# Optimization experiments

Hardware: AMD Instinct MI355X
Metric: run time of the kernel (lower is better)

## Reference

```python
import jax, jax.numpy as jnp
import numpy as np

B, LQ, LK, D = 16, 2048, 2048, 64
EPS = 1e-13
KEEP_PROB = 0.8  # fraction of key positions kept in the mask


def setup_inputs() -> dict:
    key = jax.random.key(0)
    kq, kk, kv, km = jax.random.split(key, 4)
    q = jax.random.normal(kq, (B, LQ, D), dtype=jnp.float32)
    k = jax.random.normal(kk, (B, LK, D), dtype=jnp.float32)
    v = jax.random.normal(kv, (B, LK, D), dtype=jnp.float32)
    # binary 0/1 float mask over key positions (ESIM-style padding mask)
    v_mask = (jax.random.uniform(km, (B, LK)) < KEEP_PROB).astype(jnp.float32)
    return {"q": q, "k": k, "v": v, "v_mask": v_mask}


def masked_softmax(scores, mask):
    # ESIM masked_softmax: softmax(scores * mask) * mask, renormalized.
    m = mask[:, None, :]  # [B, 1, Lk] broadcast over query dim
    p = jax.nn.softmax(scores * m, axis=-1) * m
    return p / (jnp.sum(p, axis=-1, keepdims=True) + EPS)


def reference(q, k, v, v_mask):
    scores = jnp.einsum("bqd,bkd->bqk", q, k)  # [B, Lq, Lk]
    attend = masked_softmax(scores, v_mask)
    return jnp.einsum("bqk,bkd->bqd", attend, v)  # [B, Lq, D]
```

## Files before the change

kernel.cpp:

```cpp
#include <hip/hip_runtime.h>
#include <hip/hip_bf16.h>
#include <stdint.h>

#define NB 16
#define SLQ 2048
#define SLK 2048
#define DD 64
#define BQ 128
#define BK 64
#define NT (SLK / BK)
#define QTILES (SLQ / BQ)
#define LOG2E 1.44269504f

typedef _Float16 f16x8 __attribute__((ext_vector_type(8)));
typedef short s16x8 __attribute__((ext_vector_type(8)));
typedef float f32x4 __attribute__((ext_vector_type(4)));
typedef float f32x2 __attribute__((ext_vector_type(2)));
typedef float f32x16 __attribute__((ext_vector_type(16)));

typedef __attribute__((address_space(1))) const void gvoid;
typedef __attribute__((address_space(3))) void lvoid;

__device__ __forceinline__ int swzb(int row, int bytecol) {
    return row * 128 + (bytecol ^ ((row & 7) << 4));
}
__device__ __forceinline__ int ldsq(int row, int bytecol) {
    return (row >> 6) * 8192 + swzb(row & 63, bytecol);
}

__device__ __forceinline__ void gload16(const void* g, void* l) {
    __builtin_amdgcn_global_load_lds((gvoid*)g, (lvoid*)l, 16, 0, 0);
}

__device__ __forceinline__ uint16_t f2bf(float f) {
    __bf16 h = (__bf16)f;
    return __builtin_bit_cast(uint16_t, h);
}
__device__ __forceinline__ float bf2f(uint16_t u) {
    uint32_t x = ((uint32_t)u) << 16;
    return __builtin_bit_cast(float, x);
}

__global__ __launch_bounds__(256)
void prep_all(const float* __restrict__ q, const float* __restrict__ k,
              const float* __restrict__ v, const float* __restrict__ vm,
              char* __restrict__ qs, char* __restrict__ ks,
              char* __restrict__ vts, float* __restrict__ bias2) {
    const int bid = blockIdx.x;
    if (bid < 1024) {
        const int tl = bid & 511;
        const bool isq = bid < 512;
        const float sc = isq ? LOG2E : 1.0f;
        const float* src = (isq ? q : k) + (size_t)tl * (BK * DD);
        char* dst = (isq ? qs : ks) + (size_t)tl * (BK * DD * 2);
        #pragma unroll
        for (int it = 0; it < 2; ++it) {
            int c = threadIdx.x + it * 256;
            int row = c >> 3, col8 = c & 7;
            f32x4 a  = *(const f32x4*)(src + row * DD + col8 * 8);
            f32x4 b2 = *(const f32x4*)(src + row * DD + col8 * 8 + 4);
            f16x8 h;
            #pragma unroll
            for (int j = 0; j < 4; ++j) {
                h[j] = (_Float16)(a[j] * sc);
                h[4 + j] = (_Float16)(b2[j] * sc);
            }
            *(f16x8*)(dst + swzb(row, col8 * 16)) = h;
        }
    } else if (bid < 1536) {
        const int tl = bid - 1024;
        const float* src = v + (size_t)tl * (BK * DD);
        char* dst = vts + (size_t)tl * (BK * DD * 2);
        const int d = threadIdx.x & 63;
        #pragma unroll
        for (int it = 0; it < 2; ++it) {
            int key8 = (threadIdx.x >> 6) + it * 4;
            s16x8 h;
            #pragma unroll
            for (int j = 0; j < 8; ++j)
                h[j] = (short)f2bf(src[(key8 * 8 + j) * DD + d]);
            *(s16x8*)(dst + swzb(d, key8 * 16)) = h;
        }
    } else {
        int i = (bid - 1536) * 256 + threadIdx.x;
        bias2[i] = (vm[i] != 0.f) ? 0.f : -2e30f;
    }
}

__global__ __launch_bounds__(256, 3)
void attn_fwd(const char* __restrict__ qs, const char* __restrict__ ks,
              const char* __restrict__ vts, const float* __restrict__ bias2,
              float* __restrict__ po, float* __restrict__ pl,
              float* __restrict__ out, int nsp)
{
    __shared__ __align__(16) char lp[BQ * DD * 2];
    __shared__ __align__(16) char lk[2][BK * DD * 2];
    __shared__ __align__(16) char lv[2][BK * DD * 2];

    const int tid  = threadIdx.x;
    const int lane = tid & 63;
    const int w    = tid >> 6;
    const int lh   = lane >> 5;
    const int lr   = lane & 31;

    const int G = 256 * nsp;
    int wg = blockIdx.x;
    wg = (wg & 7) * (G >> 3) + (wg >> 3);
    const int qt   = wg & 15;
    const int rest = wg >> 4;
    const int sp   = rest % nsp;
    const int b    = rest / nsp;

    const int qq = NT / nsp, rm = NT % nsp;
    const int t0  = sp * qq + (sp < rm ? sp : rm);
    const int cnt = qq + (sp < rm ? 1 : 0);

    const char* qtile = qs  + (size_t)(b * 32 + qt * 2) * 8192;
    const char* kbase = ks  + (size_t)(b * 32 + t0) * 8192;
    const char* vbase = vts + (size_t)(b * 32 + t0) * 8192;
    const float* mbias = bias2 + (size_t)b * SLK + t0 * BK;

    #pragma unroll
    for (int i = 0; i < 4; ++i) {
        int ch = w * 4 + i;
        gload16(qtile + ch * 1024 + lane * 16, lp + ch * 1024);
    }
    #pragma unroll
    for (int i = 0; i < 2; ++i) {
        int ch = w * 2 + i;
        gload16(kbase + ch * 1024 + lane * 16, lk[0] + ch * 1024);
        gload16(vbase + ch * 1024 + lane * 16, lv[0] + ch * 1024);
    }
    asm volatile("s_waitcnt vmcnt(0)" ::: "memory");
    __syncthreads();

    f16x8 qf[4];
    #pragma unroll
    for (int kd = 0; kd < 4; ++kd)
        qf[kd] = *(const f16x8*)(lp + ldsq(w * 32 + lr, kd * 32 + lh * 16));

    s16x8 ones;
    #pragma unroll
    for (int j = 0; j < 8; ++j) ones[j] = (short)0x3F80;

    f32x16 oacc0 = (f32x16)(0.0f), oacc1 = (f32x16)(0.0f), rsacc = (f32x16)(0.0f);

    int buf = 0;
    for (int kt = 0; kt < cnt; ++kt) {
        float bv0 = mbias[kt * BK + lr];
        float bv1 = mbias[kt * BK + 32 + lr];

        if (kt + 1 < cnt) {
            const char* kg = kbase + (size_t)(kt + 1) * 8192;
            const char* vg = vbase + (size_t)(kt + 1) * 8192;
            #pragma unroll
            for (int i = 0; i < 2; ++i) {
                int ch = w * 2 + i;
                gload16(kg + ch * 1024 + lane * 16, lk[buf ^ 1] + ch * 1024);
                gload16(vg + ch * 1024 + lane * 16, lv[buf ^ 1] + ch * 1024);
            }
        }

        f32x16 s0 = (f32x16)(0.0f), s1 = (f32x16)(0.0f);
        #pragma unroll
        for (int kd = 0; kd < 4; ++kd) {
            f16x8 kf0 = *(const f16x8*)(lk[buf] + swzb(lr,      kd * 32 + lh * 16));
            f16x8 kf1 = *(const f16x8*)(lk[buf] + swzb(32 + lr, kd * 32 + lh * 16));
            s0 = __builtin_amdgcn_mfma_f32_32x32x16_f16(qf[kd], kf0, s0, 0, 0, 0);
            s1 = __builtin_amdgcn_mfma_f32_32x32x16_f16(qf[kd], kf1, s1, 0, 0, 0);
        }

        #pragma unroll
        for (int r = 0; r < 16; ++r) {
            int row = w * 32 + (r & 3) + 8 * (r >> 2) + 4 * lh;
            float p0 = exp2f(s0[r] + bv0);
            float p1 = exp2f(s1[r] + bv1);
            *(uint16_t*)(lp + ldsq(row, lr * 2))      = f2bf(p0);
            *(uint16_t*)(lp + ldsq(row, 64 + lr * 2)) = f2bf(p1);
        }

        s16x8 pa[4];
        #pragma unroll
        for (int kk = 0; kk < 4; ++kk) {
            pa[kk] = *(const s16x8*)(lp + ldsq(w * 32 + lr, kk * 32 + lh * 16));
            rsacc = __builtin_amdgcn_mfma_f32_32x32x16_bf16(pa[kk], ones, rsacc, 0, 0, 0);
        }
        #pragma unroll
        for (int kk = 0; kk < 4; ++kk) {
            s16x8 vf0 = *(const s16x8*)(lv[buf] + swzb(lr,      kk * 32 + lh * 16));
            s16x8 vf1 = *(const s16x8*)(lv[buf] + swzb(32 + lr, kk * 32 + lh * 16));
            oacc0 = __builtin_amdgcn_mfma_f32_32x32x16_bf16(pa[kk], vf0, oacc0, 0, 0, 0);
            oacc1 = __builtin_amdgcn_mfma_f32_32x32x16_bf16(pa[kk], vf1, oacc1, 0, 0, 0);
        }

        asm volatile("s_waitcnt vmcnt(0)" ::: "memory");
        __syncthreads();
        buf ^= 1;
    }

    if (nsp == 1) {
        float* ob = out + ((size_t)b * SLQ + (size_t)qt * BQ) * DD;
        #pragma unroll
        for (int r = 0; r < 16; ++r) {
            int row = w * 32 + (r & 3) + 8 * (r >> 2) + 4 * lh;
            float inv = 1.f / (rsacc[r] + 1e-13f);
            ob[row * DD + lr]      = oacc0[r] * inv;
            ob[row * DD + 32 + lr] = oacc1[r] * inv;
        }
    } else {
        float* pob = po + (size_t)wg * (BQ * DD);
        #pragma unroll
        for (int r = 0; r < 16; ++r) {
            int row = w * 32 + (r & 3) + 8 * (r >> 2) + 4 * lh;
            pob[row * DD + lr]      = oacc0[r];
            pob[row * DD + 32 + lr] = oacc1[r];
            if (lr == 0) pl[(size_t)wg * BQ + row] = rsacc[r];
        }
    }
}

__global__ __launch_bounds__(256)
void merge_k(const float* __restrict__ po, const float* __restrict__ pl,
             float* __restrict__ out, int nsp) {
    const int t  = blockIdx.x;
    const int b  = t >> 4, qt = t & 15;
    const int i0 = (b * nsp) * 16 + qt;
    const int r0 = threadIdx.x >> 4;
    const int c4 = (threadIdx.x & 15) * 4;
    float* ob = out + ((size_t)b * SLQ + (size_t)qt * BQ) * DD;
    for (int rr = 0; rr < BQ; rr += 16) {
        int r = r0 + rr;
        float l = 1e-13f;
        f32x4 acc = (f32x4){0.f, 0.f, 0.f, 0.f};
        for (int s = 0; s < nsp; ++s) {
            int idx = i0 + s * 16;
            l += pl[(size_t)idx * BQ + r];
            f32x4 a = *(const f32x4*)(po + (size_t)idx * (BQ * DD) + r * DD + c4);
            acc += a;
        }
        float inv = 1.f / l;
        f32x4 o;
        #pragma unroll
        for (int j = 0; j < 4; ++j) o[j] = acc[j] * inv;
        *(f32x4*)(ob + r * DD + c4) = o;
    }
}

__global__ __launch_bounds__(256, 2)
void attn_fallback(const float* __restrict__ q, const float* __restrict__ k,
                   const float* __restrict__ v, const float* __restrict__ vm,
                   float* __restrict__ out)
{
    __shared__ __align__(16) char lqh[64 * DD * 2];
    __shared__ __align__(16) char lql[64 * DD * 2];
    __shared__ __align__(16) char lkh[BK * DD * 2];
    __shared__ __align__(16) char lkl[BK * DD * 2];
    __shared__ __align__(16) char lvt[DD * BK * 2];
    __shared__ __align__(16) char lpp[64 * BK * 2];
    __shared__ float lmask[BK];

    const int tid  = threadIdx.x;
    const int lane = tid & 63;
    const int w    = tid >> 6;
    const int lg   = lane >> 4;
    const int lm   = lane & 15;

    const int b  = blockIdx.y;
    const int qt = blockIdx.x;

    const float* qb = q + ((size_t)b * SLQ + (size_t)qt * 64) * DD;
    const float* kb = k + (size_t)b * SLK * DD;
    const float* vb = v + (size_t)b * SLK * DD;
    const float* mb = vm + (size_t)b * SLK;

    #pragma unroll
    for (int it = 0; it < 2; ++it) {
        int c = tid + it * 256;
        int row = c >> 3, col8 = c & 7;
        f32x4 a  = *(const f32x4*)(qb + row * DD + col8 * 8);
        f32x4 bb = *(const f32x4*)(qb + row * DD + col8 * 8 + 4);
        s16x8 h, l;
        #pragma unroll
        for (int j = 0; j < 4; ++j) {
            uint16_t hh = f2bf(a[j]);
            h[j] = (short)hh; l[j] = (short)f2bf(a[j] - bf2f(hh));
            uint16_t hb = f2bf(bb[j]);
            h[4 + j] = (short)hb; l[4 + j] = (short)f2bf(bb[j] - bf2f(hb));
        }
        *(s16x8*)(lqh + swzb(row, col8 * 16)) = h;
        *(s16x8*)(lql + swzb(row, col8 * 16)) = l;
    }
    __syncthreads();

    s16x8 qfh[2], qfl[2];
    #pragma unroll
    for (int kc = 0; kc < 2; ++kc) {
        qfh[kc] = *(const s16x8*)(lqh + swzb(w * 16 + lm, kc * 64 + lg * 16));
        qfl[kc] = *(const s16x8*)(lql + swzb(w * 16 + lm, kc * 64 + lg * 16));
    }

    float mrow[4], lrow[4];
    f32x4 oacc[4];
    #pragma unroll
    for (int i = 0; i < 4; ++i) { mrow[i] = -1e30f; lrow[i] = 0.f; }
    #pragma unroll
    for (int d = 0; d < 4; ++d) oacc[d] = (f32x4){0.f, 0.f, 0.f, 0.f};

    for (int kt = 0; kt < NT; ++kt) {
        __syncthreads();
        const float* ks2 = kb + (size_t)kt * BK * DD;
        const float* vs = vb + (size_t)kt * BK * DD;

        #pragma unroll
        for (int it = 0; it < 2; ++it) {
            int c = tid + it * 256;
            int row = c >> 3, col8 = c & 7;
            f32x4 a  = *(const f32x4*)(ks2 + row * DD + col8 * 8);
            f32x4 bb = *(const f32x4*)(ks2 + row * DD + col8 * 8 + 4);
            s16x8 h, l;
            #pragma unroll
            for (int j = 0; j < 4; ++j) {
                uint16_t hh = f2bf(a[j]);
                h[j] = (short)hh; l[j] = (short)f2bf(a[j] - bf2f(hh));
                uint16_t hb = f2bf(bb[j]);
                h[4 + j] = (short)hb; l[4 + j] = (short)f2bf(bb[j] - bf2f(hb));
            }
            *(s16x8*)(lkh + swzb(row, col8 * 16)) = h;
            *(s16x8*)(lkl + swzb(row, col8 * 16)) = l;
        }
        #pragma unroll
        for (int it = 0; it < 8; ++it) {
            int c = tid + it * 256;
            int key = c >> 5, dp = (c & 31) * 2;
            f32x2 a = *(const f32x2*)(vs + key * DD + dp);
            *(uint16_t*)(lvt + swzb(dp,     key * 2)) = f2bf(a[0]);
            *(uint16_t*)(lvt + swzb(dp + 1, key * 2)) = f2bf(a[1]);
        }
        if (tid < BK) lmask[tid] = mb[kt * BK + tid];
        __syncthreads();

        f32x4 s[4];
        #pragma unroll
        for (int f = 0; f < 4; ++f) s[f] = (f32x4){0.f, 0.f, 0.f, 0.f};
        #pragma unroll
        for (int f = 0; f < 4; ++f) {
            #pragma unroll
            for (int kc = 0; kc < 2; ++kc) {
                s16x8 kfh = *(const s16x8*)(lkh + swzb(f * 16 + lm, kc * 64 + lg * 16));
                s16x8 kfl = *(const s16x8*)(lkl + swzb(f * 16 + lm, kc * 64 + lg * 16));
                s[f] = __builtin_amdgcn_mfma_f32_16x16x32_bf16(qfh[kc], kfh, s[f], 0, 0, 0);
                s[f] = __builtin_amdgcn_mfma_f32_16x16x32_bf16(qfh[kc], kfl, s[f], 0, 0, 0);
                s[f] = __builtin_amdgcn_mfma_f32_16x16x32_bf16(qfl[kc], kfh, s[f], 0, 0, 0);
            }
        }

        float mv[4];
        #pragma unroll
        for (int f = 0; f < 4; ++f) mv[f] = lmask[f * 16 + lm];

        float pmax[4];
        #pragma unroll
        for (int i = 0; i < 4; ++i) {
            float x = -1e30f;
            #pragma unroll
            for (int f = 0; f < 4; ++f) {
                float sv = (mv[f] != 0.f) ? s[f][i] : -1e30f;
                s[f][i] = sv;
                x = fmaxf(x, sv);
            }
            #pragma unroll
            for (int off = 1; off < 16; off <<= 1)
                x = fmaxf(x, __shfl_xor(x, off, 64));
            pmax[i] = x;
        }

        float scl[4];
        #pragma unroll
        for (int i = 0; i < 4; ++i) {
            float mn = fmaxf(mrow[i], pmax[i]);
            scl[i] = __expf(mrow[i] - mn);
            mrow[i] = mn;
        }
        float rs[4] = {0.f, 0.f, 0.f, 0.f};
        #pragma unroll
        for (int f = 0; f < 4; ++f) {
            #pragma unroll
            for (int i = 0; i < 4; ++i) {
                float p = __expf(s[f][i] - mrow[i]);
                s[f][i] = p;
                rs[i] += p;
            }
        }
        #pragma unroll
        for (int i = 0; i < 4; ++i) {
            #pragma unroll
            for (int off = 1; off < 16; off <<= 1)
                rs[i] += __shfl_xor(rs[i], off, 64);
            lrow[i] = lrow[i] * scl[i] + rs[i];
        }
        #pragma unroll
        for (int d = 0; d < 4; ++d)
            #pragma unroll
            for (int i = 0; i < 4; ++i)
                oacc[d][i] *= scl[i];

        #pragma unroll
        for (int f = 0; f < 4; ++f)
            #pragma unroll
            for (int i = 0; i < 4; ++i)
                *(uint16_t*)(lpp + swzb(w * 16 + lg * 4 + i, (f * 16 + lm) * 2)) = f2bf(s[f][i]);
        __syncthreads();

        #pragma unroll
        for (int kc = 0; kc < 2; ++kc) {
            s16x8 pf = *(const s16x8*)(lpp + swzb(w * 16 + lm, kc * 64 + lg * 16));
            #pragma unroll
            for (int d = 0; d < 4; ++d) {
                s16x8 vf = *(const s16x8*)(lvt + swzb(d * 16 + lm, kc * 64 + lg * 16));
                oacc[d] = __builtin_amdgcn_mfma_f32_16x16x32_bf16(pf, vf, oacc[d], 0, 0, 0);
            }
        }
    }

    float* ob = out + ((size_t)b * SLQ + (size_t)qt * 64) * DD;
    #pragma unroll
    for (int i = 0; i < 4; ++i) {
        float inv = 1.f / (lrow[i] + 1e-13f);
        int row = w * 16 + lg * 4 + i;
        #pragma unroll
        for (int d = 0; d < 4; ++d)
            ob[row * DD + d * 16 + lm] = oacc[d][i] * inv;
    }
}

extern "C" void kernel_launch(void* const* d_in, const int* in_sizes, int n_in,
                              void* d_out, int out_size, void* d_ws, size_t ws_size,
                              hipStream_t stream) {
    const float* q  = (const float*)d_in[0];
    const float* k  = (const float*)d_in[1];
    const float* v  = (const float*)d_in[2];
    const float* vm = (const float*)d_in[3];
    float* out = (float*)d_out;

    const size_t TB     = (size_t)NB * SLK * DD * 2;
    const size_t BIAS   = (size_t)NB * SLK * 4;
    const size_t PL_PER = (size_t)NB * QTILES * BQ * 4;
    const size_t PO_PER = (size_t)NB * QTILES * BQ * DD * 4;
    const size_t base = 3 * TB + BIAS;

    int nsp = 0;
    for (int c = 3; c >= 1; --c) {
        if (ws_size >= base + (size_t)c * (PL_PER + PO_PER)) { nsp = c; break; }
    }
    if (nsp == 0) {
        if (ws_size >= base) nsp = 1;
        else {
            dim3 grid(SLQ / 64, NB);
            attn_fallback<<<grid, dim3(256), 0, stream>>>(q, k, v, vm, out);
            return;
        }
    }

    char*  qs    = (char*)d_ws;
    char*  ks    = qs + TB;
    char*  vts   = ks + TB;
    float* bias2 = (float*)(vts + TB);
    float* pl    = (float*)((char*)bias2 + BIAS);
    float* po    = (float*)((char*)pl + (size_t)nsp * PL_PER);

    prep_all<<<dim3(1664), dim3(256), 0, stream>>>(q, k, v, vm, qs, ks, vts, bias2);
    attn_fwd<<<dim3(256 * nsp), dim3(256), 0, stream>>>(qs, ks, vts, bias2, po, pl, out, nsp);
    if (nsp > 1)
        merge_k<<<dim3(NB * QTILES), dim3(256), 0, stream>>>(po, pl, out, nsp);
}
```

Baseline: 56.16 us.

## Keep softmax probabilities in registers and apply mask via V zeroing and rowsum

Swaps the QK^T MFMA operand order so the score accumulator layout can be fed straight back as the A operand of the PV MFMA, which removes the LDS round trip for the probability tile. The key mask is no longer added as a bias before exp. Masked keys are zeroed in the bf16 V copy, and the row-sum MFMA multiplies by a bf16 mask vector instead of ones. Keys are permuted within groups of 16 (sigma16) so the register layout lines up, which adds more index arithmetic to the prep kernel.

```diff
diff --git a/kernel.cpp b/kernel.cpp
--- a/kernel.cpp
+++ b/kernel.cpp
@@ -14,6 +14,8 @@
 
 typedef _Float16 f16x8 __attribute__((ext_vector_type(8)));
 typedef short s16x8 __attribute__((ext_vector_type(8)));
+typedef unsigned int u32x4 __attribute__((ext_vector_type(4)));
+typedef unsigned short u16x4 __attribute__((ext_vector_type(4)));
 typedef float f32x4 __attribute__((ext_vector_type(4)));
 typedef float f32x2 __attribute__((ext_vector_type(2)));
 typedef float f32x16 __attribute__((ext_vector_type(16)));
@@ -39,13 +41,31 @@
 __device__ __forceinline__ float bf2f(uint16_t u) {
     uint32_t x = ((uint32_t)u) << 16;
     return __builtin_bit_cast(float, x);
+}
+
+__device__ __forceinline__ int sigma16(int x) {
+    return (x & ~12) | ((x & 4) << 1) | ((x & 8) >> 1);
+}
+
+__device__ __forceinline__ void build_pa(const f32x16& s, s16x8& paA, s16x8& paB) {
+    uint32_t w[8];
+    #pragma unroll
+    for (int i = 0; i < 8; ++i) {
+        float p0 = exp2f(s[2 * i]);
+        float p1 = exp2f(s[2 * i + 1]);
+        w[i] = (uint32_t)f2bf(p0) | ((uint32_t)f2bf(p1) << 16);
+    }
+    u32x4 wa = {w[0], w[1], w[2], w[3]};
+    u32x4 wb = {w[4], w[5], w[6], w[7]};
+    paA = __builtin_bit_cast(s16x8, wa);
+    paB = __builtin_bit_cast(s16x8, wb);
 }
 
 __global__ __launch_bounds__(256)
 void prep_all(const float* __restrict__ q, const float* __restrict__ k,
               const float* __restrict__ v, const float* __restrict__ vm,
               char* __restrict__ qs, char* __restrict__ ks,
-              char* __restrict__ vts, float* __restrict__ bias2) {
+              char* __restrict__ vts, uint16_t* __restrict__ mb16) {
     const int bid = blockIdx.x;
     if (bid < 1024) {
         const int tl = bid & 511;
@@ -70,6 +90,7 @@
     } else if (bid < 1536) {
         const int tl = bid - 1024;
         const float* src = v + (size_t)tl * (BK * DD);
+        const float* msk = vm + (size_t)tl * BK;
         char* dst = vts + (size_t)tl * (BK * DD * 2);
         const int d = threadIdx.x & 63;
         #pragma unroll
@@ -77,23 +98,32 @@
             int key8 = (threadIdx.x >> 6) + it * 4;
             s16x8 h;
             #pragma unroll
-            for (int j = 0; j < 8; ++j)
-                h[j] = (short)f2bf(src[(key8 * 8 + j) * DD + d]);
+            for (int j = 0; j < 8; ++j) {
+                int kp = key8 * 8 + j;
+                int sk = (kp & ~15) | sigma16(kp & 15);
+                float mv = msk[sk];
+                h[j] = (short)f2bf((mv != 0.f) ? src[sk * DD + d] : 0.f);
+            }
             *(s16x8*)(dst + swzb(d, key8 * 16)) = h;
         }
     } else {
-        int i = (bid - 1536) * 256 + threadIdx.x;
-        bias2[i] = (vm[i] != 0.f) ? 0.f : -2e30f;
+        int i = (bid - 1536) * 1024 + threadIdx.x * 4;
+        f32x4 m = *(const f32x4*)(vm + i);
+        u16x4 o;
+        #pragma unroll
+        for (int j = 0; j < 4; ++j) o[j] = (m[j] != 0.f) ? (uint16_t)0x3F80 : (uint16_t)0;
+        int pos = (i & ~15) | sigma16(i & 15);
+        *(u16x4*)(mb16 + pos) = o;
     }
 }
 
 __global__ __launch_bounds__(256, 3)
 void attn_fwd(const char* __restrict__ qs, const char* __restrict__ ks,
-              const char* __restrict__ vts, const float* __restrict__ bias2,
+              const char* __restrict__ vts, const uint16_t* __restrict__ mb16,
               float* __restrict__ po, float* __restrict__ pl,
               float* __restrict__ out, int nsp)
 {
-    __shared__ __align__(16) char lp[BQ * DD * 2];
+    __shared__ __align__(16) char lq[BQ * DD * 2];
     __shared__ __align__(16) char lk[2][BK * DD * 2];
     __shared__ __align__(16) char lv[2][BK * DD * 2];
 
@@ -118,12 +148,12 @@
     const char* qtile = qs  + (size_t)(b * 32 + qt * 2) * 8192;
     const char* kbase = ks  + (size_t)(b * 32 + t0) * 8192;
     const char* vbase = vts + (size_t)(b * 32 + t0) * 8192;
-    const float* mbias = bias2 + (size_t)b * SLK + t0 * BK;
+    const uint16_t* mkbase = mb16 + (size_t)b * SLK + t0 * BK;
 
     #pragma unroll
     for (int i = 0; i < 4; ++i) {
         int ch = w * 4 + i;
-        gload16(qtile + ch * 1024 + lane * 16, lp + ch * 1024);
+        gload16(qtile + ch * 1024 + lane * 16, lq + ch * 1024);
     }
     #pragma unroll
     for (int i = 0; i < 2; ++i) {
@@ -137,18 +167,16 @@
     f16x8 qf[4];
     #pragma unroll
     for (int kd = 0; kd < 4; ++kd)
-        qf[kd] = *(const f16x8*)(lp + ldsq(w * 32 + lr, kd * 32 + lh * 16));
-
-    s16x8 ones;
-    #pragma unroll
-    for (int j = 0; j < 8; ++j) ones[j] = (short)0x3F80;
+        qf[kd] = *(const f16x8*)(lq + ldsq(w * 32 + lr, kd * 32 + lh * 16));
 
     f32x16 oacc0 = (f32x16)(0.0f), oacc1 = (f32x16)(0.0f), rsacc = (f32x16)(0.0f);
 
     int buf = 0;
     for (int kt = 0; kt < cnt; ++kt) {
-        float bv0 = mbias[kt * BK + lr];
-        float bv1 = mbias[kt * BK + 32 + lr];
+        s16x8 mf[4];
+        #pragma unroll
+        for (int kk = 0; kk < 4; ++kk)
+            mf[kk] = *(const s16x8*)(mkbase + kt * BK + kk * 16 + lh * 8);
 
         if (kt + 1 < cnt) {
             const char* kg = kbase + (size_t)(kt + 1) * 8192;
@@ -166,25 +194,18 @@
         for (int kd = 0; kd < 4; ++kd) {
             f16x8 kf0 = *(const f16x8*)(lk[buf] + swzb(lr,      kd * 32 + lh * 16));
             f16x8 kf1 = *(const f16x8*)(lk[buf] + swzb(32 + lr, kd * 32 + lh * 16));
-            s0 = __builtin_amdgcn_mfma_f32_32x32x16_f16(qf[kd], kf0, s0, 0, 0, 0);
-            s1 = __builtin_amdgcn_mfma_f32_32x32x16_f16(qf[kd], kf1, s1, 0, 0, 0);
-        }
-
-        #pragma unroll
-        for (int r = 0; r < 16; ++r) {
-            int row = w * 32 + (r & 3) + 8 * (r >> 2) + 4 * lh;
-            float p0 = exp2f(s0[r] + bv0);
-            float p1 = exp2f(s1[r] + bv1);
-            *(uint16_t*)(lp + ldsq(row, lr * 2))      = f2bf(p0);
-            *(uint16_t*)(lp + ldsq(row, 64 + lr * 2)) = f2bf(p1);
+            s0 = __builtin_amdgcn_mfma_f32_32x32x16_f16(kf0, qf[kd], s0, 0, 0, 0);
+            s1 = __builtin_amdgcn_mfma_f32_32x32x16_f16(kf1, qf[kd], s1, 0, 0, 0);
         }
 
         s16x8 pa[4];
-        #pragma unroll
-        for (int kk = 0; kk < 4; ++kk) {
-            pa[kk] = *(const s16x8*)(lp + ldsq(w * 32 + lr, kk * 32 + lh * 16));
-            rsacc = __builtin_amdgcn_mfma_f32_32x32x16_bf16(pa[kk], ones, rsacc, 0, 0, 0);
-        }
+        build_pa(s0, pa[0], pa[1]);
+        build_pa(s1, pa[2], pa[3]);
+
+        #pragma unroll
+        for (int kk = 0; kk < 4; ++kk)
+            rsacc = __builtin_amdgcn_mfma_f32_32x32x16_bf16(pa[kk], mf[kk], rsacc, 0, 0, 0);
+
         #pragma unroll
         for (int kk = 0; kk < 4; ++kk) {
             s16x8 vf0 = *(const s16x8*)(lv[buf] + swzb(lr,      kk * 32 + lh * 16));
@@ -443,10 +464,10 @@
     float* out = (float*)d_out;
 
     const size_t TB     = (size_t)NB * SLK * DD * 2;
-    const size_t BIAS   = (size_t)NB * SLK * 4;
+    const size_t MB     = (size_t)NB * SLK * 2;
     const size_t PL_PER = (size_t)NB * QTILES * BQ * 4;
     const size_t PO_PER = (size_t)NB * QTILES * BQ * DD * 4;
-    const size_t base = 3 * TB + BIAS;
+    const size_t base = 3 * TB + MB;
 
     int nsp = 0;
     for (int c = 3; c >= 1; --c) {
@@ -461,15 +482,15 @@
         }
     }
 
-    char*  qs    = (char*)d_ws;
-    char*  ks    = qs + TB;
-    char*  vts   = ks + TB;
-    float* bias2 = (float*)(vts + TB);
-    float* pl    = (float*)((char*)bias2 + BIAS);
-    float* po    = (float*)((char*)pl + (size_t)nsp * PL_PER);
-
-    prep_all<<<dim3(1664), dim3(256), 0, stream>>>(q, k, v, vm, qs, ks, vts, bias2);
-    attn_fwd<<<dim3(256 * nsp), dim3(256), 0, stream>>>(qs, ks, vts, bias2, po, pl, out, nsp);
+    char*     qs   = (char*)d_ws;
+    char*     ks   = qs + TB;
+    char*     vts  = ks + TB;
+    uint16_t* mb16 = (uint16_t*)(vts + TB);
+    float*    pl   = (float*)((char*)mb16 + MB);
+    float*    po   = (float*)((char*)pl + (size_t)nsp * PL_PER);
+
+    prep_all<<<dim3(1568), dim3(256), 0, stream>>>(q, k, v, vm, qs, ks, vts, mb16);
+    attn_fwd<<<dim3(256 * nsp), dim3(256), 0, stream>>>(qs, ks, vts, mb16, po, pl, out, nsp);
     if (nsp > 1)
         merge_k<<<dim3(NB * QTILES), dim3(256), 0, stream>>>(po, pl, out, nsp);
 }
```

Measured after the change: 57.23 us. No clear change (+1.9%).

## Halve query tile to 64 rows using 16x16x32 MFMA and bf16 split partials

Applied to the files above, without the earlier changes.

The attention kernel now uses 64-row query tiles, with each wave handling 16 rows via 16x16x32 MFMA instructions instead of 32x32x16. The grid is twice as large, occupancy is raised to 4 blocks, and split-K partial outputs are stored in bf16 to cut merge traffic. The maximum split count drops from 3 to 2. The aim is more parallelism and less partial-output bandwidth, at the cost of re-reading K/V tiles for twice as many query blocks and a small loss of precision in partials.

```diff
diff --git a/kernel.cpp b/kernel.cpp
--- a/kernel.cpp
+++ b/kernel.cpp
@@ -6,7 +6,7 @@
 #define SLQ 2048
 #define SLK 2048
 #define DD 64
-#define BQ 128
+#define BQ 64
 #define BK 64
 #define NT (SLK / BK)
 #define QTILES (SLQ / BQ)
@@ -14,18 +14,15 @@
 
 typedef _Float16 f16x8 __attribute__((ext_vector_type(8)));
 typedef short s16x8 __attribute__((ext_vector_type(8)));
+typedef unsigned short u16x4 __attribute__((ext_vector_type(4)));
 typedef float f32x4 __attribute__((ext_vector_type(4)));
 typedef float f32x2 __attribute__((ext_vector_type(2)));
-typedef float f32x16 __attribute__((ext_vector_type(16)));
 
 typedef __attribute__((address_space(1))) const void gvoid;
 typedef __attribute__((address_space(3))) void lvoid;
 
 __device__ __forceinline__ int swzb(int row, int bytecol) {
     return row * 128 + (bytecol ^ ((row & 7) << 4));
-}
-__device__ __forceinline__ int ldsq(int row, int bytecol) {
-    return (row >> 6) * 8192 + swzb(row & 63, bytecol);
 }
 
 __device__ __forceinline__ void gload16(const void* g, void* l) {
@@ -87,10 +84,10 @@
     }
 }
 
-__global__ __launch_bounds__(256, 3)
+__global__ __launch_bounds__(256, 4)
 void attn_fwd(const char* __restrict__ qs, const char* __restrict__ ks,
               const char* __restrict__ vts, const float* __restrict__ bias2,
-              float* __restrict__ po, float* __restrict__ pl,
+              uint16_t* __restrict__ po, float* __restrict__ pl,
               float* __restrict__ out, int nsp)
 {
     __shared__ __align__(16) char lp[BQ * DD * 2];
@@ -100,14 +97,14 @@
     const int tid  = threadIdx.x;
     const int lane = tid & 63;
     const int w    = tid >> 6;
-    const int lh   = lane >> 5;
-    const int lr   = lane & 31;
-
-    const int G = 256 * nsp;
+    const int lg   = lane >> 4;
+    const int lm   = lane & 15;
+
+    const int G = 512 * nsp;
     int wg = blockIdx.x;
     wg = (wg & 7) * (G >> 3) + (wg >> 3);
-    const int qt   = wg & 15;
-    const int rest = wg >> 4;
+    const int qt   = wg & 31;
+    const int rest = wg >> 5;
     const int sp   = rest % nsp;
     const int b    = rest / nsp;
 
@@ -115,14 +112,14 @@
     const int t0  = sp * qq + (sp < rm ? sp : rm);
     const int cnt = qq + (sp < rm ? 1 : 0);
 
-    const char* qtile = qs  + (size_t)(b * 32 + qt * 2) * 8192;
+    const char* qtile = qs  + (size_t)(b * 32 + qt) * 8192;
     const char* kbase = ks  + (size_t)(b * 32 + t0) * 8192;
     const char* vbase = vts + (size_t)(b * 32 + t0) * 8192;
     const float* mbias = bias2 + (size_t)b * SLK + t0 * BK;
 
     #pragma unroll
-    for (int i = 0; i < 4; ++i) {
-        int ch = w * 4 + i;
+    for (int i = 0; i < 2; ++i) {
+        int ch = w * 2 + i;
         gload16(qtile + ch * 1024 + lane * 16, lp + ch * 1024);
     }
     #pragma unroll
@@ -134,21 +131,25 @@
     asm volatile("s_waitcnt vmcnt(0)" ::: "memory");
     __syncthreads();
 
-    f16x8 qf[4];
-    #pragma unroll
-    for (int kd = 0; kd < 4; ++kd)
-        qf[kd] = *(const f16x8*)(lp + ldsq(w * 32 + lr, kd * 32 + lh * 16));
+    f16x8 qf[2];
+    #pragma unroll
+    for (int kc = 0; kc < 2; ++kc)
+        qf[kc] = *(const f16x8*)(lp + swzb(w * 16 + lm, kc * 64 + lg * 16));
 
     s16x8 ones;
     #pragma unroll
     for (int j = 0; j < 8; ++j) ones[j] = (short)0x3F80;
 
-    f32x16 oacc0 = (f32x16)(0.0f), oacc1 = (f32x16)(0.0f), rsacc = (f32x16)(0.0f);
+    f32x4 oacc[4], rsacc;
+    #pragma unroll
+    for (int d = 0; d < 4; ++d) oacc[d] = (f32x4){0.f, 0.f, 0.f, 0.f};
+    rsacc = (f32x4){0.f, 0.f, 0.f, 0.f};
 
     int buf = 0;
     for (int kt = 0; kt < cnt; ++kt) {
-        float bv0 = mbias[kt * BK + lr];
-        float bv1 = mbias[kt * BK + 32 + lr];
+        float bv[4];
+        #pragma unroll
+        for (int f = 0; f < 4; ++f) bv[f] = mbias[kt * BK + f * 16 + lm];
 
         if (kt + 1 < cnt) {
             const char* kg = kbase + (size_t)(kt + 1) * 8192;
@@ -161,36 +162,36 @@
             }
         }
 
-        f32x16 s0 = (f32x16)(0.0f), s1 = (f32x16)(0.0f);
-        #pragma unroll
-        for (int kd = 0; kd < 4; ++kd) {
-            f16x8 kf0 = *(const f16x8*)(lk[buf] + swzb(lr,      kd * 32 + lh * 16));
-            f16x8 kf1 = *(const f16x8*)(lk[buf] + swzb(32 + lr, kd * 32 + lh * 16));
-            s0 = __builtin_amdgcn_mfma_f32_32x32x16_f16(qf[kd], kf0, s0, 0, 0, 0);
-            s1 = __builtin_amdgcn_mfma_f32_32x32x16_f16(qf[kd], kf1, s1, 0, 0, 0);
-        }
-
-        #pragma unroll
-        for (int r = 0; r < 16; ++r) {
-            int row = w * 32 + (r & 3) + 8 * (r >> 2) + 4 * lh;
-            float p0 = exp2f(s0[r] + bv0);
-            float p1 = exp2f(s1[r] + bv1);
-            *(uint16_t*)(lp + ldsq(row, lr * 2))      = f2bf(p0);
-            *(uint16_t*)(lp + ldsq(row, 64 + lr * 2)) = f2bf(p1);
-        }
-
-        s16x8 pa[4];
-        #pragma unroll
-        for (int kk = 0; kk < 4; ++kk) {
-            pa[kk] = *(const s16x8*)(lp + ldsq(w * 32 + lr, kk * 32 + lh * 16));
-            rsacc = __builtin_amdgcn_mfma_f32_32x32x16_bf16(pa[kk], ones, rsacc, 0, 0, 0);
-        }
-        #pragma unroll
-        for (int kk = 0; kk < 4; ++kk) {
-            s16x8 vf0 = *(const s16x8*)(lv[buf] + swzb(lr,      kk * 32 + lh * 16));
-            s16x8 vf1 = *(const s16x8*)(lv[buf] + swzb(32 + lr, kk * 32 + lh * 16));
-            oacc0 = __builtin_amdgcn_mfma_f32_32x32x16_bf16(pa[kk], vf0, oacc0, 0, 0, 0);
-            oacc1 = __builtin_amdgcn_mfma_f32_32x32x16_bf16(pa[kk], vf1, oacc1, 0, 0, 0);
+        f32x4 s[4];
+        #pragma unroll
+        for (int f = 0; f < 4; ++f) s[f] = (f32x4){0.f, 0.f, 0.f, 0.f};
+        #pragma unroll
+        for (int f = 0; f < 4; ++f) {
+            #pragma unroll
+            for (int kc = 0; kc < 2; ++kc) {
+                f16x8 kf = *(const f16x8*)(lk[buf] + swzb(f * 16 + lm, kc * 64 + lg * 16));
+                s[f] = __builtin_amdgcn_mfma_f32_16x16x32_f16(qf[kc], kf, s[f], 0, 0, 0);
+            }
+        }
+
+        #pragma unroll
+        for (int f = 0; f < 4; ++f) {
+            #pragma unroll
+            for (int i = 0; i < 4; ++i) {
+                float p = __builtin_amdgcn_exp2f(s[f][i] + bv[f]);
+                *(uint16_t*)(lp + swzb(w * 16 + lg * 4 + i, (f * 16 + lm) * 2)) = f2bf(p);
+            }
+        }
+
+        #pragma unroll
+        for (int kc = 0; kc < 2; ++kc) {
+            s16x8 pf = *(const s16x8*)(lp + swzb(w * 16 + lm, kc * 64 + lg * 16));
+            rsacc = __builtin_amdgcn_mfma_f32_16x16x32_bf16(pf, ones, rsacc, 0, 0, 0);
+            #pragma unroll
+            for (int d = 0; d < 4; ++d) {
+                s16x8 vf = *(const s16x8*)(lv[buf] + swzb(d * 16 + lm, kc * 64 + lg * 16));
+                oacc[d] = __builtin_amdgcn_mfma_f32_16x16x32_bf16(pf, vf, oacc[d], 0, 0, 0);
+            }
         }
 
         asm volatile("s_waitcnt vmcnt(0)" ::: "memory");
@@ -201,42 +202,46 @@
     if (nsp == 1) {
         float* ob = out + ((size_t)b * SLQ + (size_t)qt * BQ) * DD;
         #pragma unroll
-        for (int r = 0; r < 16; ++r) {
-            int row = w * 32 + (r & 3) + 8 * (r >> 2) + 4 * lh;
-            float inv = 1.f / (rsacc[r] + 1e-13f);
-            ob[row * DD + lr]      = oacc0[r] * inv;
-            ob[row * DD + 32 + lr] = oacc1[r] * inv;
+        for (int i = 0; i < 4; ++i) {
+            float inv = 1.f / (rsacc[i] + 1e-13f);
+            int row = w * 16 + lg * 4 + i;
+            #pragma unroll
+            for (int d = 0; d < 4; ++d)
+                ob[row * DD + d * 16 + lm] = oacc[d][i] * inv;
         }
     } else {
-        float* pob = po + (size_t)wg * (BQ * DD);
-        #pragma unroll
-        for (int r = 0; r < 16; ++r) {
-            int row = w * 32 + (r & 3) + 8 * (r >> 2) + 4 * lh;
-            pob[row * DD + lr]      = oacc0[r];
-            pob[row * DD + 32 + lr] = oacc1[r];
-            if (lr == 0) pl[(size_t)wg * BQ + row] = rsacc[r];
+        uint16_t* pob = po + (size_t)wg * (BQ * DD);
+        #pragma unroll
+        for (int i = 0; i < 4; ++i) {
+            int row = w * 16 + lg * 4 + i;
+            #pragma unroll
+            for (int d = 0; d < 4; ++d)
+                pob[row * DD + d * 16 + lm] = f2bf(oacc[d][i]);
+            if (lm == 0) pl[(size_t)wg * BQ + row] = rsacc[i];
         }
     }
 }
 
 __global__ __launch_bounds__(256)
-void merge_k(const float* __restrict__ po, const float* __restrict__ pl,
+void merge_k(const uint16_t* __restrict__ po, const float* __restrict__ pl,
              float* __restrict__ out, int nsp) {
     const int t  = blockIdx.x;
-    const int b  = t >> 4, qt = t & 15;
-    const int i0 = (b * nsp) * 16 + qt;
+    const int b  = t >> 5, qt = t & 31;
+    const int i0 = (b * nsp) * 32 + qt;
     const int r0 = threadIdx.x >> 4;
     const int c4 = (threadIdx.x & 15) * 4;
     float* ob = out + ((size_t)b * SLQ + (size_t)qt * BQ) * DD;
+    #pragma unroll
     for (int rr = 0; rr < BQ; rr += 16) {
         int r = r0 + rr;
         float l = 1e-13f;
         f32x4 acc = (f32x4){0.f, 0.f, 0.f, 0.f};
         for (int s = 0; s < nsp; ++s) {
-            int idx = i0 + s * 16;
+            int idx = i0 + s * 32;
             l += pl[(size_t)idx * BQ + r];
-            f32x4 a = *(const f32x4*)(po + (size_t)idx * (BQ * DD) + r * DD + c4);
-            acc += a;
+            u16x4 a = *(const u16x4*)(po + (size_t)idx * (BQ * DD) + r * DD + c4);
+            #pragma unroll
+            for (int j = 0; j < 4; ++j) acc[j] += bf2f(a[j]);
         }
         float inv = 1.f / l;
         f32x4 o;
@@ -445,11 +450,11 @@
     const size_t TB     = (size_t)NB * SLK * DD * 2;
     const size_t BIAS   = (size_t)NB * SLK * 4;
     const size_t PL_PER = (size_t)NB * QTILES * BQ * 4;
-    const size_t PO_PER = (size_t)NB * QTILES * BQ * DD * 4;
+    const size_t PO_PER = (size_t)NB * QTILES * BQ * DD * 2;
     const size_t base = 3 * TB + BIAS;
 
     int nsp = 0;
-    for (int c = 3; c >= 1; --c) {
+    for (int c = 2; c >= 1; --c) {
         if (ws_size >= base + (size_t)c * (PL_PER + PO_PER)) { nsp = c; break; }
     }
     if (nsp == 0) {
@@ -461,15 +466,15 @@
         }
     }
 
-    char*  qs    = (char*)d_ws;
-    char*  ks    = qs + TB;
-    char*  vts   = ks + TB;
-    float* bias2 = (float*)(vts + TB);
-    float* pl    = (float*)((char*)bias2 + BIAS);
-    float* po    = (float*)((char*)pl + (size_t)nsp * PL_PER);
+    char*     qs    = (char*)d_ws;
+    char*     ks    = qs + TB;
+    char*     vts   = ks + TB;
+    float*    bias2 = (float*)(vts + TB);
+    float*    pl    = (float*)((char*)bias2 + BIAS);
+    uint16_t* po    = (uint16_t*)((char*)pl + (size_t)nsp * PL_PER);
 
     prep_all<<<dim3(1664), dim3(256), 0, stream>>>(q, k, v, vm, qs, ks, vts, bias2);
-    attn_fwd<<<dim3(256 * nsp), dim3(256), 0, stream>>>(qs, ks, vts, bias2, po, pl, out, nsp);
+    attn_fwd<<<dim3(512 * nsp), dim3(256), 0, stream>>>(qs, ks, vts, bias2, po, pl, out, nsp);
     if (nsp > 1)
         merge_k<<<dim3(NB * QTILES), dim3(256), 0, stream>>>(po, pl, out, nsp);
 }
```

Measured after the change: 49.15 us, median of 2. 12.5% less time.
